# Optimization experiments

Measured on AMD Instinct MI355X. Metric: run time of the kernel, lower is better.

## Reference

```python
import jax, jax.numpy as jnp
import numpy as np

N = 50000
E = 800000
IN_DIM = 256
HID = 128
HEADS = 2
OUT_DIM = 256
NEG_SLOPE = 0.2  # DGL GATConv default


def gat_layer(x, W, a_l, a_r, b, src, dst, num_nodes):
    """One DGL-style GATConv layer (eval mode, no dropout).
    x: [N, Fin]; W: [Fin, heads*d]; a_l, a_r: [heads, d]; b: [heads, d].
    Returns [N, heads, d].
    """
    heads, d = a_l.shape
    z = (x @ W).reshape(num_nodes, heads, d)              # [N, heads, d]
    el = jnp.einsum('nhd,hd->nh', z, a_l)                 # [N, heads]
    er = jnp.einsum('nhd,hd->nh', z, a_r)                 # [N, heads]
    e = el[src] + er[dst]                                 # [E, heads]
    e = jnp.where(e > 0, e, NEG_SLOPE * e)                # LeakyReLU
    # segment softmax over incoming edges of each dst node
    m = jax.ops.segment_max(e, dst, num_segments=num_nodes)   # [N, heads]
    ex = jnp.exp(e - m[dst])                               # [E, heads]
    s = jax.ops.segment_sum(ex, dst, num_segments=num_nodes)  # [N, heads]
    alpha = ex / s[dst]                                    # [E, heads]
    # weighted scatter-add aggregation
    msg = z[src] * alpha[:, :, None]                       # [E, heads, d]
    out = jax.ops.segment_sum(msg, dst, num_segments=num_nodes)  # [N, heads, d]
    return out + b[None, :, :]


def setup_inputs() -> dict:
    key = jax.random.key(0)
    ks = jax.random.split(key, 12)
    sc1 = 1.0 / np.sqrt(IN_DIM)
    sc2 = 1.0 / np.sqrt(HEADS * HID)
    return {
        'node_feats': jax.random.normal(ks[0], (N, IN_DIM), dtype=jnp.float32),
        'src': jax.random.randint(ks[1], (E,), 0, N, dtype=jnp.int32),
        'dst': jax.random.randint(ks[2], (E,), 0, N, dtype=jnp.int32),
        'W1': jax.random.normal(ks[3], (IN_DIM, HEADS * HID), dtype=jnp.float32) * sc1,
        'al1': jax.random.normal(ks[4], (HEADS, HID), dtype=jnp.float32) * sc1,
        'ar1': jax.random.normal(ks[5], (HEADS, HID), dtype=jnp.float32) * sc1,
        'b1': jnp.zeros((HEADS, HID), dtype=jnp.float32),
        'W2': jax.random.normal(ks[6], (HEADS * HID, OUT_DIM), dtype=jnp.float32) * sc2,
        'al2': jax.random.normal(ks[7], (1, OUT_DIM), dtype=jnp.float32) * sc2,
        'ar2': jax.random.normal(ks[8], (1, OUT_DIM), dtype=jnp.float32) * sc2,
        'b2': jnp.zeros((1, OUT_DIM), dtype=jnp.float32),
    }


def reference(node_feats, src, dst, W1, al1, ar1, b1, W2, al2, ar2, b2):
    h = gat_layer(node_feats, W1, al1, ar1, b1, src, dst, N)   # [N, heads, HID]
    h = jax.nn.relu(h.reshape(N, HEADS * HID))                 # flatten(1) + relu
    out = gat_layer(h, W2, al2, ar2, b2, src, dst, N)          # [N, 1, OUT_DIM]
    return out[:, 0, :]                                        # squeeze(1)
```

## Files before the change

kernel.cpp:

```cpp
#include <hip/hip_runtime.h>
#include <hip/hip_fp16.h>
#include <math.h>


typedef _Float16 half8 __attribute__((ext_vector_type(8)));
typedef float floatx4 __attribute__((ext_vector_type(4)));

__device__ __forceinline__ float rl_f(float x, int i) {
  return __int_as_float(__builtin_amdgcn_readlane(__float_as_int(x), i));
}
__device__ __forceinline__ unsigned pk2(float a, float b) {
  return (unsigned)__half_as_ushort(__float2half_rn(a)) |
         ((unsigned)__half_as_ushort(__float2half_rn(b)) << 16);
}

__device__ __forceinline__ void fma_row(float4& acc, uint2 zv, float e) {
  union { uint2 u; __half h[4]; } w;
  w.u = zv;
  acc.x = fmaf(__half2float(w.h[0]), e, acc.x);
  acc.y = fmaf(__half2float(w.h[1]), e, acc.y);
  acc.z = fmaf(__half2float(w.h[2]), e, acc.z);
  acc.w = fmaf(__half2float(w.h[3]), e, acc.w);
}

__global__ __launch_bounds__(256) void zero_f4(float4* __restrict__ p, int n4) {
  int i = blockIdx.x * 256 + threadIdx.x;
  if (i < n4) p[i] = make_float4(0.f, 0.f, 0.f, 0.f);
}

__global__ __launch_bounds__(256) void cvt_half(const float4* __restrict__ in,
                                                uint2* __restrict__ outh, int n4) {
  int i = blockIdx.x * 256 + threadIdx.x;
  if (i < n4) {
    float4 v = in[i];
    uint2 o;
    o.x = pk2(v.x, v.y);
    o.y = pk2(v.z, v.w);
    outh[i] = o;
  }
}

__global__ __launch_bounds__(256) void transpose_w2(const float* __restrict__ W1,
                                                    const float* __restrict__ W2,
                                                    unsigned short* __restrict__ w1t,
                                                    unsigned short* __restrict__ w2t) {
  int b = blockIdx.x;
  const float* W = (b < 256) ? W1 : W2;
  unsigned short* Wt = (b < 256) ? w1t : w2t;
  int k = b & 255, n = threadIdx.x;
  Wt[n * 256 + k] = __half_as_ushort(__float2half_rn(W[k * 256 + n]));
}

__global__ __launch_bounds__(256) void hist_dst(const int* __restrict__ dst,
                                                int* __restrict__ counts, int E) {
  int i = blockIdx.x * 256 + threadIdx.x;
  if (i < E) atomicAdd(&counts[dst[i]], 1);
}

__global__ __launch_bounds__(256) void scan_block(const int* __restrict__ counts,
                                                  int* __restrict__ offsets,
                                                  int* __restrict__ bsum, int Nn) {
  __shared__ int sm[256];
  int t = threadIdx.x;
  int i = blockIdx.x * 256 + t;
  int v = (i < Nn) ? counts[i] : 0;
  sm[t] = v;
  __syncthreads();
  for (int off = 1; off < 256; off <<= 1) {
    int x = (t >= off) ? sm[t - off] : 0;
    __syncthreads();
    sm[t] += x;
    __syncthreads();
  }
  if (i < Nn) offsets[i] = sm[t] - v;
  if (t == 255) bsum[blockIdx.x] = sm[255];
}

__global__ __launch_bounds__(256) void scan_bsum(int* __restrict__ bsum,
                                                 int* __restrict__ bofs, int B) {
  __shared__ int sm[256];
  int t = threadIdx.x;
  int v = (t < B) ? bsum[t] : 0;
  sm[t] = v;
  __syncthreads();
  for (int off = 1; off < 256; off <<= 1) {
    int x = (t >= off) ? sm[t - off] : 0;
    __syncthreads();
    sm[t] += x;
    __syncthreads();
  }
  if (t < B) bofs[t] = sm[t] - v;
}

__global__ __launch_bounds__(256) void scan_add(int* __restrict__ offsets,
                                                const int* __restrict__ bofs,
                                                int* __restrict__ cursor, int Nn) {
  int i = blockIdx.x * 256 + threadIdx.x;
  if (i < Nn) {
    int o = offsets[i] + bofs[i >> 8];
    offsets[i] = o;
    cursor[i] = o;
  }
}

__global__ __launch_bounds__(256) void scatter_edges(const int* __restrict__ src,
                                                     const int* __restrict__ dst,
                                                     int* __restrict__ cursor,
                                                     int* __restrict__ esrc, int E) {
  int i = blockIdx.x * 256 + threadIdx.x;
  if (i < E) {
    int pos = atomicAdd(&cursor[dst[i]], 1);
    esrc[pos] = src[i];
  }
}

template <int HS>
__global__ __launch_bounds__(256, 2) void gemm_mfma(const unsigned short* __restrict__ A,
                                                    const unsigned short* __restrict__ Wt,
                                                    unsigned short* __restrict__ C,
                                                    const float* __restrict__ al,
                                                    const float* __restrict__ ar,
                                                    float* __restrict__ el,
                                                    float* __restrict__ er, int M) {
  const int tid = threadIdx.x;
  const int wv = tid >> 6, lane = tid & 63;
  const int ln = lane & 15, kg = lane >> 4;

  half8 bf[8][4];
#pragma unroll
  for (int kb = 0; kb < 8; kb++)
#pragma unroll
    for (int t = 0; t < 4; t++)
      bf[kb][t] = *(const half8*)(Wt + (size_t)((4 * wv + t) * 16 + ln) * 256 +
                                  kb * 32 + kg * 8);

  const int cb = wv * 64 + kg * 4;
  float4 av[4], rv[4];
#pragma unroll
  for (int t = 0; t < 4; t++) {
    av[t] = *(const float4*)(al + cb + t * 16);
    rv[t] = *(const float4*)(ar + cb + t * 16);
  }

  const int nchunk = (M + 15) >> 4;
  for (int c = blockIdx.x; c < nchunk; c += gridDim.x) {
    const int m0 = c << 4;
    const int row = m0 + ln;
    const unsigned short* ap = A + (size_t)((row < M) ? row : (M - 1)) * 256 + kg * 8;

    half8 af[8];
#pragma unroll
    for (int kb = 0; kb < 8; kb++) af[kb] = *(const half8*)(ap + kb * 32);

    floatx4 acc[4];
#pragma unroll
    for (int t = 0; t < 4; t++) acc[t] = (floatx4)0.f;

#pragma unroll
    for (int kb = 0; kb < 8; kb++)
#pragma unroll
      for (int t = 0; t < 4; t++)
        acc[t] = __builtin_amdgcn_mfma_f32_16x16x32_f16(bf[kb][t], af[kb], acc[t], 0, 0, 0);

    float pl = 0.f, pr = 0.f;
#pragma unroll
    for (int t = 0; t < 4; t++) {
      pl += acc[t].x * av[t].x + acc[t].y * av[t].y + acc[t].z * av[t].z + acc[t].w * av[t].w;
      pr += acc[t].x * rv[t].x + acc[t].y * rv[t].y + acc[t].z * rv[t].z + acc[t].w * rv[t].w;
    }
    pl += __shfl_xor(pl, 16); pl += __shfl_xor(pl, 32);
    pr += __shfl_xor(pr, 16); pr += __shfl_xor(pr, 32);

    if (row < M) {
      if (lane < 16) {
        const int idx = HS ? (row * 2 + (wv >> 1)) : row;
        atomicAdd(&el[idx], pl);
        atomicAdd(&er[idx], pr);
      }
      unsigned short* cp = C + (size_t)row * 256 + wv * 64 + kg * 4;
#pragma unroll
      for (int t = 0; t < 4; t++) {
        uint2 o;
        o.x = pk2(acc[t].x, acc[t].y);
        o.y = pk2(acc[t].z, acc[t].w);
        *(uint2*)(cp + t * 16) = o;
      }
    }
  }
}

template <int HS, int RELU, int OUTH>
__global__ __launch_bounds__(256) void node_aggregate(const unsigned short* __restrict__ z,
                                                      const float* __restrict__ el,
                                                      const float* __restrict__ er,
                                                      const int* __restrict__ esrc,
                                                      const int* __restrict__ offsets,
                                                      const int* __restrict__ counts,
                                                      const float* __restrict__ bias,
                                                      void* __restrict__ out, int Nn) {
  int n = (blockIdx.x * 256 + threadIdx.x) >> 6;
  int lane = threadIdx.x & 63;
  if (n >= Nn) return;
  const int beg = offsets[n];
  const int deg = counts[n];
  float ern0, ern1 = 0.f;
  if (HS) {
    float2 e = ((const float2*)er)[n];
    ern0 = e.x; ern1 = e.y;
  } else {
    ern0 = er[n];
  }
  const int head = HS ? (lane >> 5) : 0;

  float s0 = 0.f, s1 = 0.f;
  float4 acc = make_float4(0.f, 0.f, 0.f, 0.f);
  const uint2* zp = (const uint2*)z;

  for (int base = 0; base < deg; base += 64) {
    const int cnt = min(64, deg - base);
    int sn = 0;
    float myex0 = 0.f, myex1 = 0.f;
    if (lane < cnt) {
      sn = esrc[beg + base + lane];
      if (HS) {
        float2 elv = ((const float2*)el)[sn];
        float v0 = elv.x + ern0; v0 = (v0 > 0.f) ? v0 : 0.2f * v0;
        float v1 = elv.y + ern1; v1 = (v1 > 0.f) ? v1 : 0.2f * v1;
        myex0 = __expf(v0);
        myex1 = __expf(v1);
      } else {
        float v0 = el[sn] + ern0; v0 = (v0 > 0.f) ? v0 : 0.2f * v0;
        myex0 = __expf(v0);
      }
      s0 += myex0;
      s1 += myex1;
    }

    int i = 0;
    for (; i + 8 <= cnt; i += 8) {
      int s_[8];
      float e_[8];
      uint2 zv[8];
#pragma unroll
      for (int j = 0; j < 8; j++) {
        s_[j] = __builtin_amdgcn_readlane(sn, i + j);
        float e0 = rl_f(myex0, i + j);
        if (HS) {
          float e1 = rl_f(myex1, i + j);
          e_[j] = head ? e1 : e0;
        } else {
          e_[j] = e0;
        }
      }
#pragma unroll
      for (int j = 0; j < 8; j++) zv[j] = zp[((size_t)s_[j] << 6) + lane];
#pragma unroll
      for (int j = 0; j < 8; j++) fma_row(acc, zv[j], e_[j]);
    }
    for (; i < cnt; i++) {
      int si = __builtin_amdgcn_readlane(sn, i);
      float e = rl_f(myex0, i);
      if (HS) {
        float e1 = rl_f(myex1, i);
        if (head) e = e1;
      }
      uint2 zv = zp[((size_t)si << 6) + lane];
      fma_row(acc, zv, e);
    }
  }

#pragma unroll
  for (int o = 32; o > 0; o >>= 1) {
    s0 += __shfl_xor(s0, o);
    if (HS) s1 += __shfl_xor(s1, o);
  }
  const float s = (HS && head) ? s1 : s0;
  float4 bb = ((const float4*)bias)[lane];
  float4 v;
  if (deg > 0) {
    float inv = 1.f / s;
    v = make_float4(acc.x * inv + bb.x, acc.y * inv + bb.y,
                    acc.z * inv + bb.z, acc.w * inv + bb.w);
  } else {
    v = bb;
  }
  if (RELU) {
    v.x = fmaxf(v.x, 0.f); v.y = fmaxf(v.y, 0.f);
    v.z = fmaxf(v.z, 0.f); v.w = fmaxf(v.w, 0.f);
  }
  if (OUTH) {
    uint2 o;
    o.x = pk2(v.x, v.y);
    o.y = pk2(v.z, v.w);
    ((uint2*)out)[((size_t)n << 6) + lane] = o;
  } else {
    ((float4*)out)[((size_t)n << 6) + lane] = v;
  }
}

extern "C" void kernel_launch(void* const* d_in, const int* in_sizes, int n_in,
                              void* d_out, int out_size, void* d_ws, size_t ws_size,
                              hipStream_t stream) {
  const float* x   = (const float*)d_in[0];
  const int*   src = (const int*)d_in[1];
  const int*   dst = (const int*)d_in[2];
  const float* W1  = (const float*)d_in[3];
  const float* al1 = (const float*)d_in[4];
  const float* ar1 = (const float*)d_in[5];
  const float* b1  = (const float*)d_in[6];
  const float* W2  = (const float*)d_in[7];
  const float* al2 = (const float*)d_in[8];
  const float* ar2 = (const float*)d_in[9];
  const float* b2  = (const float*)d_in[10];
  float* out = (float*)d_out;
  (void)n_in; (void)out_size; (void)ws_size;

  const int Nn = in_sizes[0] / 256;
  const int Ee = in_sizes[1];
  const int F = 256;
  const int NB = (Nn + 255) / 256;

  unsigned short* z   = (unsigned short*)d_ws;
  unsigned short* xh  = z + (size_t)Nn * F;
  unsigned short* w1t = xh + (size_t)Nn * F;
  unsigned short* w2t = w1t + 65536;
  int*   esrc   = (int*)(w2t + 65536);
  int*   counts = esrc + Ee;
  int*   offs   = counts + Nn;
  int*   cursor = offs + Nn;
  int*   bsum   = cursor + Nn;
  int*   bofs   = bsum + 256;
  float* el1p   = (float*)(bofs + 256);
  float* er1p   = el1p + (size_t)Nn * 2;
  float* el2p   = er1p + (size_t)Nn * 2;
  float* er2p   = el2p + Nn;

  dim3 blk(256);

  cvt_half<<<(Nn * 64 + 255) / 256, blk, 0, stream>>>((const float4*)x, (uint2*)xh, Nn * 64);
  transpose_w2<<<512, blk, 0, stream>>>(W1, W2, w1t, w2t);

  const int zn4 = (9 * Nn + 512) / 4;
  zero_f4<<<(zn4 + 255) / 256, blk, 0, stream>>>((float4*)counts, zn4);

  hist_dst<<<(Ee + 255) / 256, blk, 0, stream>>>(dst, counts, Ee);
  scan_block<<<NB, blk, 0, stream>>>(counts, offs, bsum, Nn);
  scan_bsum<<<1, blk, 0, stream>>>(bsum, bofs, NB);
  scan_add<<<NB, blk, 0, stream>>>(offs, bofs, cursor, Nn);
  scatter_edges<<<(Ee + 255) / 256, blk, 0, stream>>>(src, dst, cursor, esrc, Ee);

  const int gemm_grid = 512;

  gemm_mfma<1><<<gemm_grid, blk, 0, stream>>>(xh, w1t, z, al1, ar1, el1p, er1p, Nn);
  node_aggregate<1, 1, 1><<<(Nn + 3) / 4, blk, 0, stream>>>(z, el1p, er1p, esrc, offs,
                                                            counts, b1, xh, Nn);

  gemm_mfma<0><<<gemm_grid, blk, 0, stream>>>(xh, w2t, z, al2, ar2, el2p, er2p, Nn);
  node_aggregate<0, 0, 0><<<(Nn + 3) / 4, blk, 0, stream>>>(z, el2p, er2p, esrc, offs,
                                                            counts, b2, out, Nn);
}
```

Before: 380.5 us.

## Fuse fp32-to-half conversion into GEMM and process two edges per wave in aggregation

The standalone cvt_half kernel is removed, and the first GEMM now reads fp32 node features directly and converts them to half in registers. The node aggregation kernel is restructured so each half-wave handles a different edge, with each lane loading 16 bytes (8 halves) instead of 8. The two half-wave partial sums are combined with a cross-lane shuffle. This aims to remove a full read/write pass over the input and to double per-lane gather width with fewer row iterations, at the cost of extra readlanes, selects and shuffles and a more complex odd-edge tail.

Result: slower. 411.2 us (+8.1%).

```diff
diff --git a/kernel.cpp b/kernel.cpp
--- a/kernel.cpp
+++ b/kernel.cpp
@@ -14,30 +14,16 @@
          ((unsigned)__half_as_ushort(__float2half_rn(b)) << 16);
 }
 
-__device__ __forceinline__ void fma_row(float4& acc, uint2 zv, float e) {
-  union { uint2 u; __half h[4]; } w;
+__device__ __forceinline__ void fma_row8(float* acc, uint4 zv, float e) {
+  union { uint4 u; __half h[8]; } w;
   w.u = zv;
-  acc.x = fmaf(__half2float(w.h[0]), e, acc.x);
-  acc.y = fmaf(__half2float(w.h[1]), e, acc.y);
-  acc.z = fmaf(__half2float(w.h[2]), e, acc.z);
-  acc.w = fmaf(__half2float(w.h[3]), e, acc.w);
+#pragma unroll
+  for (int k = 0; k < 8; k++) acc[k] = fmaf(__half2float(w.h[k]), e, acc[k]);
 }
 
 __global__ __launch_bounds__(256) void zero_f4(float4* __restrict__ p, int n4) {
   int i = blockIdx.x * 256 + threadIdx.x;
   if (i < n4) p[i] = make_float4(0.f, 0.f, 0.f, 0.f);
-}
-
-__global__ __launch_bounds__(256) void cvt_half(const float4* __restrict__ in,
-                                                uint2* __restrict__ outh, int n4) {
-  int i = blockIdx.x * 256 + threadIdx.x;
-  if (i < n4) {
-    float4 v = in[i];
-    uint2 o;
-    o.x = pk2(v.x, v.y);
-    o.y = pk2(v.z, v.w);
-    outh[i] = o;
-  }
 }
 
 __global__ __launch_bounds__(256) void transpose_w2(const float* __restrict__ W1,
@@ -114,8 +100,8 @@
   }
 }
 
-template <int HS>
-__global__ __launch_bounds__(256, 2) void gemm_mfma(const unsigned short* __restrict__ A,
+template <int HS, int AF32>
+__global__ __launch_bounds__(256, 2) void gemm_mfma(const void* __restrict__ Av,
                                                     const unsigned short* __restrict__ Wt,
                                                     unsigned short* __restrict__ C,
                                                     const float* __restrict__ al,
@@ -146,11 +132,27 @@
   for (int c = blockIdx.x; c < nchunk; c += gridDim.x) {
     const int m0 = c << 4;
     const int row = m0 + ln;
-    const unsigned short* ap = A + (size_t)((row < M) ? row : (M - 1)) * 256 + kg * 8;
+    const int rr = (row < M) ? row : (M - 1);
 
     half8 af[8];
-#pragma unroll
-    for (int kb = 0; kb < 8; kb++) af[kb] = *(const half8*)(ap + kb * 32);
+    if (AF32) {
+      const float* ap = (const float*)Av + (size_t)rr * 256 + kg * 8;
+#pragma unroll
+      for (int kb = 0; kb < 8; kb++) {
+        float4 u0 = *(const float4*)(ap + kb * 32);
+        float4 u1 = *(const float4*)(ap + kb * 32 + 4);
+        half8 h;
+        h[0] = (_Float16)u0.x; h[1] = (_Float16)u0.y;
+        h[2] = (_Float16)u0.z; h[3] = (_Float16)u0.w;
+        h[4] = (_Float16)u1.x; h[5] = (_Float16)u1.y;
+        h[6] = (_Float16)u1.z; h[7] = (_Float16)u1.w;
+        af[kb] = h;
+      }
+    } else {
+      const unsigned short* ap = (const unsigned short*)Av + (size_t)rr * 256 + kg * 8;
+#pragma unroll
+      for (int kb = 0; kb < 8; kb++) af[kb] = *(const half8*)(ap + kb * 32);
+    }
 
     floatx4 acc[4];
 #pragma unroll
@@ -203,6 +205,10 @@
   if (n >= Nn) return;
   const int beg = offsets[n];
   const int deg = counts[n];
+  const int lo = lane & 31;
+  const int hf = lane >> 5;
+  const int hd = HS ? ((lane >> 4) & 1) : 0;
+
   float ern0, ern1 = 0.f;
   if (HS) {
     float2 e = ((const float2*)er)[n];
@@ -210,11 +216,10 @@
   } else {
     ern0 = er[n];
   }
-  const int head = HS ? (lane >> 5) : 0;
 
   float s0 = 0.f, s1 = 0.f;
-  float4 acc = make_float4(0.f, 0.f, 0.f, 0.f);
-  const uint2* zp = (const uint2*)z;
+  float acc[8] = {0.f, 0.f, 0.f, 0.f, 0.f, 0.f, 0.f, 0.f};
+  const uint4* zp = (const uint4*)z;
 
   for (int base = 0; base < deg; base += 64) {
     const int cnt = min(64, deg - base);
@@ -237,64 +242,113 @@
     }
 
     int i = 0;
-    for (; i + 8 <= cnt; i += 8) {
+    for (; i + 16 <= cnt; i += 16) {
       int s_[8];
-      float e_[8];
-      uint2 zv[8];
+      float c_[8];
+      uint4 zv[8];
 #pragma unroll
       for (int j = 0; j < 8; j++) {
-        s_[j] = __builtin_amdgcn_readlane(sn, i + j);
-        float e0 = rl_f(myex0, i + j);
+        const int ia = i + 2 * j, ib = ia + 1;
+        int sA = __builtin_amdgcn_readlane(sn, ia);
+        int sB = __builtin_amdgcn_readlane(sn, ib);
+        s_[j] = hf ? sB : sA;
+        float eA, eB;
         if (HS) {
-          float e1 = rl_f(myex1, i + j);
-          e_[j] = head ? e1 : e0;
+          float e0A = rl_f(myex0, ia), e1A = rl_f(myex1, ia);
+          float e0B = rl_f(myex0, ib), e1B = rl_f(myex1, ib);
+          eA = hd ? e1A : e0A;
+          eB = hd ? e1B : e0B;
         } else {
-          e_[j] = e0;
+          eA = rl_f(myex0, ia);
+          eB = rl_f(myex0, ib);
         }
-      }
-#pragma unroll
-      for (int j = 0; j < 8; j++) zv[j] = zp[((size_t)s_[j] << 6) + lane];
-#pragma unroll
-      for (int j = 0; j < 8; j++) fma_row(acc, zv[j], e_[j]);
-    }
-    for (; i < cnt; i++) {
-      int si = __builtin_amdgcn_readlane(sn, i);
-      float e = rl_f(myex0, i);
+        c_[j] = hf ? eB : eA;
+      }
+#pragma unroll
+      for (int j = 0; j < 8; j++) zv[j] = zp[((size_t)s_[j] << 5) + lo];
+#pragma unroll
+      for (int j = 0; j < 8; j++) fma_row8(acc, zv[j], c_[j]);
+    }
+    for (; i + 2 <= cnt; i += 2) {
+      int sA = __builtin_amdgcn_readlane(sn, i);
+      int sB = __builtin_amdgcn_readlane(sn, i + 1);
+      int s = hf ? sB : sA;
+      float eA, eB;
       if (HS) {
-        float e1 = rl_f(myex1, i);
-        if (head) e = e1;
-      }
-      uint2 zv = zp[((size_t)si << 6) + lane];
-      fma_row(acc, zv, e);
-    }
-  }
+        float e0A = rl_f(myex0, i), e1A = rl_f(myex1, i);
+        float e0B = rl_f(myex0, i + 1), e1B = rl_f(myex1, i + 1);
+        eA = hd ? e1A : e0A;
+        eB = hd ? e1B : e0B;
+      } else {
+        eA = rl_f(myex0, i);
+        eB = rl_f(myex0, i + 1);
+      }
+      float c = hf ? eB : eA;
+      uint4 zv = zp[((size_t)s << 5) + lo];
+      fma_row8(acc, zv, c);
+    }
+    if (i < cnt) {
+      int sA = __builtin_amdgcn_readlane(sn, i);
+      float eA;
+      if (HS) {
+        float e0 = rl_f(myex0, i), e1 = rl_f(myex1, i);
+        eA = hd ? e1 : e0;
+      } else {
+        eA = rl_f(myex0, i);
+      }
+      float c = hf ? 0.f : eA;
+      uint4 zv = zp[((size_t)sA << 5) + lo];
+      fma_row8(acc, zv, c);
+    }
+  }
+
+#pragma unroll
+  for (int k = 0; k < 8; k++) acc[k] += __shfl_xor(acc[k], 32);
 
 #pragma unroll
   for (int o = 32; o > 0; o >>= 1) {
     s0 += __shfl_xor(s0, o);
     if (HS) s1 += __shfl_xor(s1, o);
   }
-  const float s = (HS && head) ? s1 : s0;
-  float4 bb = ((const float4*)bias)[lane];
-  float4 v;
+  const float s = (HS && hd) ? s1 : s0;
+
+  float4 b0 = ((const float4*)bias)[2 * lo];
+  float4 b1 = ((const float4*)bias)[2 * lo + 1];
+  float vv[8];
   if (deg > 0) {
     float inv = 1.f / s;
-    v = make_float4(acc.x * inv + bb.x, acc.y * inv + bb.y,
-                    acc.z * inv + bb.z, acc.w * inv + bb.w);
+    vv[0] = acc[0] * inv + b0.x; vv[1] = acc[1] * inv + b0.y;
+    vv[2] = acc[2] * inv + b0.z; vv[3] = acc[3] * inv + b0.w;
+    vv[4] = acc[4] * inv + b1.x; vv[5] = acc[5] * inv + b1.y;
+    vv[6] = acc[6] * inv + b1.z; vv[7] = acc[7] * inv + b1.w;
   } else {
-    v = bb;
+    vv[0] = b0.x; vv[1] = b0.y; vv[2] = b0.z; vv[3] = b0.w;
+    vv[4] = b1.x; vv[5] = b1.y; vv[6] = b1.z; vv[7] = b1.w;
   }
   if (RELU) {
-    v.x = fmaxf(v.x, 0.f); v.y = fmaxf(v.y, 0.f);
-    v.z = fmaxf(v.z, 0.f); v.w = fmaxf(v.w, 0.f);
+#pragma unroll
+    for (int k = 0; k < 8; k++) vv[k] = fmaxf(vv[k], 0.f);
   }
   if (OUTH) {
-    uint2 o;
-    o.x = pk2(v.x, v.y);
-    o.y = pk2(v.z, v.w);
-    ((uint2*)out)[((size_t)n << 6) + lane] = o;
+    if (lane < 32) {
+      uint4 o;
+      o.x = pk2(vv[0], vv[1]);
+      o.y = pk2(vv[2], vv[3]);
+      o.z = pk2(vv[4], vv[5]);
+      o.w = pk2(vv[6], vv[7]);
+      ((uint4*)out)[((size_t)n << 5) + lo] = o;
+    }
   } else {
-    ((float4*)out)[((size_t)n << 6) + lane] = v;
+    float4 fa = make_float4(vv[0], vv[1], vv[2], vv[3]);
+    float4 fb = make_float4(vv[4], vv[5], vv[6], vv[7]);
+    const int sl = lane >> 1;
+    float4 ra, rb;
+    ra.x = __shfl(fa.x, sl); ra.y = __shfl(fa.y, sl);
+    ra.z = __shfl(fa.z, sl); ra.w = __shfl(fa.w, sl);
+    rb.x = __shfl(fb.x, sl); rb.y = __shfl(fb.y, sl);
+    rb.z = __shfl(fb.z, sl); rb.w = __shfl(fb.w, sl);
+    float4 w = (lane & 1) ? rb : ra;
+    ((float4*)out)[((size_t)n << 6) + lane] = w;
   }
 }
 
@@ -337,7 +391,6 @@
 
   dim3 blk(256);
 
-  cvt_half<<<(Nn * 64 + 255) / 256, blk, 0, stream>>>((const float4*)x, (uint2*)xh, Nn * 64);
   transpose_w2<<<512, blk, 0, stream>>>(W1, W2, w1t, w2t);
 
   const int zn4 = (9 * Nn + 512) / 4;
@@ -351,11 +404,11 @@
 
   const int gemm_grid = 512;
 
-  gemm_mfma<1><<<gemm_grid, blk, 0, stream>>>(xh, w1t, z, al1, ar1, el1p, er1p, Nn);
+  gemm_mfma<1, 1><<<gemm_grid, blk, 0, stream>>>(x, w1t, z, al1, ar1, el1p, er1p, Nn);
   node_aggregate<1, 1, 1><<<(Nn + 3) / 4, blk, 0, stream>>>(z, el1p, er1p, esrc, offs,
                                                             counts, b1, xh, Nn);
 
-  gemm_mfma<0><<<gemm_grid, blk, 0, stream>>>(xh, w2t, z, al2, ar2, el2p, er2p, Nn);
+  gemm_mfma<0, 0><<<gemm_grid, blk, 0, stream>>>(xh, w2t, z, al2, ar2, el2p, er2p, Nn);
   node_aggregate<0, 0, 0><<<(Nn + 3) / 4, blk, 0, stream>>>(z, el2p, er2p, esrc, offs,
                                                             counts, b2, out, Nn);
 }
```

## Fuse fp32-to-fp16 input conversion into first GEMM and unroll aggregation by 16

Applied to the files above, without the earlier changes.

Drops the separate cvt_half kernel. The first GEMM now reads fp32 node features directly and converts them to fp16 in registers, which removes one launch and the round trip of the half copy through memory. The node aggregation loop also gains a 16-edge unrolled stage ahead of the existing 8-edge one, so more gathers are in flight at once. The cost is more register pressure in both kernels and twice the load bytes per A fragment in the GEMM.

Measured after the change: 392.3 us. 1.03x slower.

```diff
diff --git a/kernel.cpp b/kernel.cpp
--- a/kernel.cpp
+++ b/kernel.cpp
@@ -26,18 +26,6 @@
 __global__ __launch_bounds__(256) void zero_f4(float4* __restrict__ p, int n4) {
   int i = blockIdx.x * 256 + threadIdx.x;
   if (i < n4) p[i] = make_float4(0.f, 0.f, 0.f, 0.f);
-}
-
-__global__ __launch_bounds__(256) void cvt_half(const float4* __restrict__ in,
-                                                uint2* __restrict__ outh, int n4) {
-  int i = blockIdx.x * 256 + threadIdx.x;
-  if (i < n4) {
-    float4 v = in[i];
-    uint2 o;
-    o.x = pk2(v.x, v.y);
-    o.y = pk2(v.z, v.w);
-    outh[i] = o;
-  }
 }
 
 __global__ __launch_bounds__(256) void transpose_w2(const float* __restrict__ W1,
@@ -114,8 +102,8 @@
   }
 }
 
-template <int HS>
-__global__ __launch_bounds__(256, 2) void gemm_mfma(const unsigned short* __restrict__ A,
+template <int HS, int AF32>
+__global__ __launch_bounds__(256, 2) void gemm_mfma(const void* __restrict__ Av,
                                                     const unsigned short* __restrict__ Wt,
                                                     unsigned short* __restrict__ C,
                                                     const float* __restrict__ al,
@@ -146,11 +134,27 @@
   for (int c = blockIdx.x; c < nchunk; c += gridDim.x) {
     const int m0 = c << 4;
     const int row = m0 + ln;
-    const unsigned short* ap = A + (size_t)((row < M) ? row : (M - 1)) * 256 + kg * 8;
+    const int rr = (row < M) ? row : (M - 1);
 
     half8 af[8];
-#pragma unroll
-    for (int kb = 0; kb < 8; kb++) af[kb] = *(const half8*)(ap + kb * 32);
+    if (AF32) {
+      const float* ap = (const float*)Av + (size_t)rr * 256 + kg * 8;
+#pragma unroll
+      for (int kb = 0; kb < 8; kb++) {
+        float4 u0 = *(const float4*)(ap + kb * 32);
+        float4 u1 = *(const float4*)(ap + kb * 32 + 4);
+        half8 h;
+        h[0] = (_Float16)u0.x; h[1] = (_Float16)u0.y;
+        h[2] = (_Float16)u0.z; h[3] = (_Float16)u0.w;
+        h[4] = (_Float16)u1.x; h[5] = (_Float16)u1.y;
+        h[6] = (_Float16)u1.z; h[7] = (_Float16)u1.w;
+        af[kb] = h;
+      }
+    } else {
+      const unsigned short* ap = (const unsigned short*)Av + (size_t)rr * 256 + kg * 8;
+#pragma unroll
+      for (int kb = 0; kb < 8; kb++) af[kb] = *(const half8*)(ap + kb * 32);
+    }
 
     floatx4 acc[4];
 #pragma unroll
@@ -237,6 +241,26 @@
     }
 
     int i = 0;
+    for (; i + 16 <= cnt; i += 16) {
+      int s_[16];
+      float e_[16];
+      uint2 zv[16];
+#pragma unroll
+      for (int j = 0; j < 16; j++) {
+        s_[j] = __builtin_amdgcn_readlane(sn, i + j);
+        float e0 = rl_f(myex0, i + j);
+        if (HS) {
+          float e1 = rl_f(myex1, i + j);
+          e_[j] = head ? e1 : e0;
+        } else {
+          e_[j] = e0;
+        }
+      }
+#pragma unroll
+      for (int j = 0; j < 16; j++) zv[j] = zp[((size_t)s_[j] << 6) + lane];
+#pragma unroll
+      for (int j = 0; j < 16; j++) fma_row(acc, zv[j], e_[j]);
+    }
     for (; i + 8 <= cnt; i += 8) {
       int s_[8];
       float e_[8];
@@ -337,7 +361,6 @@
 
   dim3 blk(256);
 
-  cvt_half<<<(Nn * 64 + 255) / 256, blk, 0, stream>>>((const float4*)x, (uint2*)xh, Nn * 64);
   transpose_w2<<<512, blk, 0, stream>>>(W1, W2, w1t, w2t);
 
   const int zn4 = (9 * Nn + 512) / 4;
@@ -351,11 +374,11 @@
 
   const int gemm_grid = 512;
 
-  gemm_mfma<1><<<gemm_grid, blk, 0, stream>>>(xh, w1t, z, al1, ar1, el1p, er1p, Nn);
+  gemm_mfma<1, 1><<<gemm_grid, blk, 0, stream>>>(x, w1t, z, al1, ar1, el1p, er1p, Nn);
   node_aggregate<1, 1, 1><<<(Nn + 3) / 4, blk, 0, stream>>>(z, el1p, er1p, esrc, offs,
                                                             counts, b1, xh, Nn);
 
-  gemm_mfma<0><<<gemm_grid, blk, 0, stream>>>(xh, w2t, z, al2, ar2, el2p, er2p, Nn);
+  gemm_mfma<0, 0><<<gemm_grid, blk, 0, stream>>>(xh, w2t, z, al2, ar2, el2p, er2p, Nn);
   node_aggregate<0, 0, 0><<<(Nn + 3) / 4, blk, 0, stream>>>(z, el2p, er2p, esrc, offs,
                                                             counts, b2, out, Nn);
 }
```

## Fuse prep kernels and double-buffer A-tile loads in MFMA GEMM

Applied to the files above, without the earlier changes.

Merges the weight transpose, workspace zeroing and fp16 conversion kernels into a single launch whose work is selected by block index. This removes two kernel launches and their gaps. The GEMM loop now prefetches the next chunk's A fragments into a second register buffer while the current chunk computes, so global load latency overlaps the MFMA work. The al/ar vectors are reloaded inside each compute step instead of being kept in registers, and the extra A buffer raises register pressure, which may hurt occupancy.

New measurement: 371.5 us. 1.02x faster.

```diff
diff --git a/kernel.cpp b/kernel.cpp
--- a/kernel.cpp
+++ b/kernel.cpp
@@ -23,32 +23,32 @@
   acc.w = fmaf(__half2float(w.h[3]), e, acc.w);
 }
 
-__global__ __launch_bounds__(256) void zero_f4(float4* __restrict__ p, int n4) {
-  int i = blockIdx.x * 256 + threadIdx.x;
-  if (i < n4) p[i] = make_float4(0.f, 0.f, 0.f, 0.f);
-}
-
-__global__ __launch_bounds__(256) void cvt_half(const float4* __restrict__ in,
-                                                uint2* __restrict__ outh, int n4) {
-  int i = blockIdx.x * 256 + threadIdx.x;
-  if (i < n4) {
-    float4 v = in[i];
-    uint2 o;
-    o.x = pk2(v.x, v.y);
-    o.y = pk2(v.z, v.w);
-    outh[i] = o;
-  }
-}
-
-__global__ __launch_bounds__(256) void transpose_w2(const float* __restrict__ W1,
-                                                    const float* __restrict__ W2,
-                                                    unsigned short* __restrict__ w1t,
-                                                    unsigned short* __restrict__ w2t) {
-  int b = blockIdx.x;
-  const float* W = (b < 256) ? W1 : W2;
-  unsigned short* Wt = (b < 256) ? w1t : w2t;
-  int k = b & 255, n = threadIdx.x;
-  Wt[n * 256 + k] = __half_as_ushort(__float2half_rn(W[k * 256 + n]));
+__global__ __launch_bounds__(256) void prep(const float* __restrict__ W1,
+                                            const float* __restrict__ W2,
+                                            unsigned short* __restrict__ w1t,
+                                            unsigned short* __restrict__ w2t,
+                                            const float4* __restrict__ x,
+                                            uint2* __restrict__ xh, int n4cvt,
+                                            float4* __restrict__ zp, int zn4, int NZ) {
+  const int b = blockIdx.x, t = threadIdx.x;
+  if (b < 512) {
+    const float* W = (b < 256) ? W1 : W2;
+    unsigned short* Wt = (b < 256) ? w1t : w2t;
+    const int k = b & 255;
+    Wt[t * 256 + k] = __half_as_ushort(__float2half_rn(W[k * 256 + t]));
+  } else if (b < 512 + NZ) {
+    const int i = (b - 512) * 256 + t;
+    if (i < zn4) zp[i] = make_float4(0.f, 0.f, 0.f, 0.f);
+  } else {
+    const int i = (b - 512 - NZ) * 256 + t;
+    if (i < n4cvt) {
+      float4 v = x[i];
+      uint2 o;
+      o.x = pk2(v.x, v.y);
+      o.y = pk2(v.z, v.w);
+      xh[i] = o;
+    }
+  }
 }
 
 __global__ __launch_bounds__(256) void hist_dst(const int* __restrict__ dst,
@@ -114,6 +114,61 @@
   }
 }
 
+
+__device__ __forceinline__ void gemm_load_a(half8* af, const unsigned short* __restrict__ A,
+                                            int row, int kg) {
+  const unsigned short* ap = A + (size_t)row * 256 + kg * 8;
+#pragma unroll
+  for (int kb = 0; kb < 8; kb++) af[kb] = *(const half8*)(ap + kb * 32);
+}
+
+template <int HS>
+__device__ __forceinline__ void gemm_compute_store(const half8 (&bf)[8][4], const half8* af,
+                                                   int m0, int lane, int ln, int kg, int wv,
+                                                   const float* __restrict__ al,
+                                                   const float* __restrict__ ar,
+                                                   float* __restrict__ el,
+                                                   float* __restrict__ er,
+                                                   unsigned short* __restrict__ C, int M) {
+  floatx4 acc[4];
+#pragma unroll
+  for (int t = 0; t < 4; t++) acc[t] = (floatx4)0.f;
+#pragma unroll
+  for (int kb = 0; kb < 8; kb++)
+#pragma unroll
+    for (int t = 0; t < 4; t++)
+      acc[t] = __builtin_amdgcn_mfma_f32_16x16x32_f16(bf[kb][t], af[kb], acc[t], 0, 0, 0);
+
+  const int cb = wv * 64 + kg * 4;
+  float pl = 0.f, pr = 0.f;
+#pragma unroll
+  for (int t = 0; t < 4; t++) {
+    float4 av = *(const float4*)(al + cb + t * 16);
+    float4 rv = *(const float4*)(ar + cb + t * 16);
+    pl += acc[t].x * av.x + acc[t].y * av.y + acc[t].z * av.z + acc[t].w * av.w;
+    pr += acc[t].x * rv.x + acc[t].y * rv.y + acc[t].z * rv.z + acc[t].w * rv.w;
+  }
+  pl += __shfl_xor(pl, 16); pl += __shfl_xor(pl, 32);
+  pr += __shfl_xor(pr, 16); pr += __shfl_xor(pr, 32);
+
+  const int row = m0 + ln;
+  if (row < M) {
+    if (lane < 16) {
+      const int idx = HS ? (row * 2 + (wv >> 1)) : row;
+      atomicAdd(&el[idx], pl);
+      atomicAdd(&er[idx], pr);
+    }
+    unsigned short* cp = C + (size_t)row * 256 + wv * 64 + kg * 4;
+#pragma unroll
+    for (int t = 0; t < 4; t++) {
+      uint2 o;
+      o.x = pk2(acc[t].x, acc[t].y);
+      o.y = pk2(acc[t].z, acc[t].w);
+      *(uint2*)(cp + t * 16) = o;
+    }
+  }
+}
+
 template <int HS>
 __global__ __launch_bounds__(256, 2) void gemm_mfma(const unsigned short* __restrict__ A,
                                                     const unsigned short* __restrict__ Wt,
@@ -134,58 +189,25 @@
       bf[kb][t] = *(const half8*)(Wt + (size_t)((4 * wv + t) * 16 + ln) * 256 +
                                   kb * 32 + kg * 8);
 
-  const int cb = wv * 64 + kg * 4;
-  float4 av[4], rv[4];
-#pragma unroll
-  for (int t = 0; t < 4; t++) {
-    av[t] = *(const float4*)(al + cb + t * 16);
-    rv[t] = *(const float4*)(ar + cb + t * 16);
-  }
-
   const int nchunk = (M + 15) >> 4;
-  for (int c = blockIdx.x; c < nchunk; c += gridDim.x) {
-    const int m0 = c << 4;
-    const int row = m0 + ln;
-    const unsigned short* ap = A + (size_t)((row < M) ? row : (M - 1)) * 256 + kg * 8;
-
-    half8 af[8];
-#pragma unroll
-    for (int kb = 0; kb < 8; kb++) af[kb] = *(const half8*)(ap + kb * 32);
-
-    floatx4 acc[4];
-#pragma unroll
-    for (int t = 0; t < 4; t++) acc[t] = (floatx4)0.f;
-
-#pragma unroll
-    for (int kb = 0; kb < 8; kb++)
-#pragma unroll
-      for (int t = 0; t < 4; t++)
-        acc[t] = __builtin_amdgcn_mfma_f32_16x16x32_f16(bf[kb][t], af[kb], acc[t], 0, 0, 0);
-
-    float pl = 0.f, pr = 0.f;
-#pragma unroll
-    for (int t = 0; t < 4; t++) {
-      pl += acc[t].x * av[t].x + acc[t].y * av[t].y + acc[t].z * av[t].z + acc[t].w * av[t].w;
-      pr += acc[t].x * rv[t].x + acc[t].y * rv[t].y + acc[t].z * rv[t].z + acc[t].w * rv[t].w;
-    }
-    pl += __shfl_xor(pl, 16); pl += __shfl_xor(pl, 32);
-    pr += __shfl_xor(pr, 16); pr += __shfl_xor(pr, 32);
-
-    if (row < M) {
-      if (lane < 16) {
-        const int idx = HS ? (row * 2 + (wv >> 1)) : row;
-        atomicAdd(&el[idx], pl);
-        atomicAdd(&er[idx], pr);
-      }
-      unsigned short* cp = C + (size_t)row * 256 + wv * 64 + kg * 4;
-#pragma unroll
-      for (int t = 0; t < 4; t++) {
-        uint2 o;
-        o.x = pk2(acc[t].x, acc[t].y);
-        o.y = pk2(acc[t].z, acc[t].w);
-        *(uint2*)(cp + t * 16) = o;
-      }
-    }
+  const int stride = gridDim.x;
+  int c0 = blockIdx.x;
+  if (c0 >= nchunk) return;
+
+  half8 af0[8], af1[8];
+  gemm_load_a(af0, A, min(c0 * 16 + ln, M - 1), kg);
+  int c1 = c0 + stride;
+
+  for (;;) {
+    if (c1 < nchunk) gemm_load_a(af1, A, min(c1 * 16 + ln, M - 1), kg);
+    gemm_compute_store<HS>(bf, af0, c0 << 4, lane, ln, kg, wv, al, ar, el, er, C, M);
+    if (c1 >= nchunk) break;
+    const int c2 = c1 + stride;
+    if (c2 < nchunk) gemm_load_a(af0, A, min(c2 * 16 + ln, M - 1), kg);
+    gemm_compute_store<HS>(bf, af1, c1 << 4, lane, ln, kg, wv, al, ar, el, er, C, M);
+    if (c2 >= nchunk) break;
+    c0 = c2;
+    c1 = c2 + stride;
   }
 }
 
@@ -337,11 +359,12 @@
 
   dim3 blk(256);
 
-  cvt_half<<<(Nn * 64 + 255) / 256, blk, 0, stream>>>((const float4*)x, (uint2*)xh, Nn * 64);
-  transpose_w2<<<512, blk, 0, stream>>>(W1, W2, w1t, w2t);
-
   const int zn4 = (9 * Nn + 512) / 4;
-  zero_f4<<<(zn4 + 255) / 256, blk, 0, stream>>>((float4*)counts, zn4);
+  const int NZ = (zn4 + 255) / 256;
+  const int n4cvt = Nn * 64;
+  const int NC = (n4cvt + 255) / 256;
+  prep<<<512 + NZ + NC, blk, 0, stream>>>(W1, W2, w1t, w2t, (const float4*)x,
+                                          (uint2*)xh, n4cvt, (float4*)counts, zn4, NZ);
 
   hist_dst<<<(Ee + 255) / 256, blk, 0, stream>>>(dst, counts, Ee);
   scan_block<<<NB, blk, 0, stream>>>(counts, offs, bsum, Nn);
```
